# Kernel optimization log

Hardware: AMD Instinct MI355X
Metric: run time of the kernel (lower is better)

The kernel has to match this reference:

```python
import jax, jax.numpy as jnp
import numpy as np

N_NODES = 50000
N_EDGES = 600000
D = 128
EPS = 1e-5


def setup_inputs() -> dict:
    key = jax.random.key(0)
    ks = jax.random.split(key, 12)
    s = 1.0 / np.sqrt(D)
    return {
        "h": jax.random.normal(ks[0], (N_NODES, D), dtype=jnp.float32),
        "src": jax.random.randint(ks[1], (N_EDGES,), 0, N_NODES),
        "dst": jax.random.randint(ks[2], (N_EDGES,), 0, N_NODES),
        "W_pre": jax.random.uniform(ks[3], (D, D), jnp.float32, -s, s),
        "b_pre": jax.random.uniform(ks[4], (D,), jnp.float32, -s, s),
        "W1": jax.random.uniform(ks[5], (D, D), jnp.float32, -s, s),
        "b1": jax.random.uniform(ks[6], (D,), jnp.float32, -s, s),
        "W2": jax.random.uniform(ks[7], (D, D), jnp.float32, -s, s),
        "b2": jax.random.uniform(ks[8], (D,), jnp.float32, -s, s),
        "gamma": jnp.ones((D,), jnp.float32),
        "beta": jnp.zeros((D,), jnp.float32),
    }


def layer_norm(x, gamma, beta):
    mu = jnp.mean(x, axis=-1, keepdims=True)
    var = jnp.mean(jnp.square(x - mu), axis=-1, keepdims=True)
    return (x - mu) * jax.lax.rsqrt(var + EPS) * gamma + beta


def reference(h, src, dst, W_pre, b_pre, W1, b1, W2, b2, gamma, beta):
    # pre-projection: [N, D]
    h = h @ W_pre + b_pre
    # message passing: gather from src, segment-sum at dst (copy_u + sum)
    agg = jax.ops.segment_sum(h[src], dst, num_segments=N_NODES)
    # MLP (dropout is identity in eval)
    h_new = jax.nn.relu(jax.nn.relu(agg @ W1 + b1) @ W2 + b2)
    # residual + LayerNorm
    return layer_norm(h + h_new, gamma, beta)
```

## Files before the change

### kernel.cpp

```cpp
#include <hip/hip_runtime.h>

#define D 128
#define EPS 1e-5f
#define SCAN_CHUNK 1024
#define TSTRIDE 136

typedef __attribute__((ext_vector_type(8))) short bf16x8;
typedef __attribute__((ext_vector_type(4))) float floatx4;

__device__ __forceinline__ unsigned short f2bf(float f) {
    union { float f; unsigned u; } v; v.f = f;
    unsigned r = v.u + 0x7fffu + ((v.u >> 16) & 1u);
    return (unsigned short)(r >> 16);
}
__device__ __forceinline__ float bf2f(unsigned short s) {
    union { unsigned u; float f; } v; v.u = ((unsigned)s) << 16; return v.f;
}

__global__ __launch_bounds__(256) void prep(const float* __restrict__ W0,
                                            const float* __restrict__ W1,
                                            const float* __restrict__ W2,
                                            unsigned short* __restrict__ wt,
                                            int* __restrict__ counts,
                                            int* __restrict__ offsets, int nN, int nE) {
    int idx = blockIdx.x * 256 + threadIdx.x;
    if (idx < 3 * D * D) {
        int w = idx >> 14;
        int r = idx & (D * D - 1);
        int f = r >> 7, k = r & (D - 1);
        const float* W = (w == 0) ? W0 : (w == 1) ? W1 : W2;
        wt[(size_t)w * D * D + (size_t)f * D + k] = f2bf(W[(size_t)k * D + f]);
    }
    if (idx < nN) counts[idx] = 0;
    if (idx == 0) offsets[nN] = nE;
}

__global__ __launch_bounds__(256) void hist_dst(const int* __restrict__ dst,
                                                int* __restrict__ counts, int nE) {
    int e = blockIdx.x * 256 + threadIdx.x;
    if (e < nE) atomicAdd(&counts[dst[e]], 1);
}

__global__ __launch_bounds__(256) void scan_chunk_sums(const int* __restrict__ counts,
                                                       int* __restrict__ chunkSums, int n) {
    __shared__ int sh[256];
    const int t = threadIdx.x;
    const int base = blockIdx.x * SCAN_CHUNK + t * 4;
    int s = 0;
#pragma unroll
    for (int i = 0; i < 4; ++i) {
        int idx = base + i;
        if (idx < n) s += counts[idx];
    }
    sh[t] = s;
    __syncthreads();
    for (int off = 128; off > 0; off >>= 1) {
        if (t < off) sh[t] += sh[t + off];
        __syncthreads();
    }
    if (t == 0) chunkSums[blockIdx.x] = sh[0];
}

__global__ __launch_bounds__(256) void scan_final(const int* __restrict__ counts,
                                                  const int* __restrict__ chunkSums,
                                                  int nChunks,
                                                  int* __restrict__ offsets,
                                                  int* __restrict__ cursor, int n) {
    __shared__ int sh[256];
    __shared__ int sbase;
    const int t = threadIdx.x;
    if (t < 64) {
        int orig = (t < nChunks) ? chunkSums[t] : 0;
        int v = orig;
#pragma unroll
        for (int off = 1; off < 64; off <<= 1) {
            int u = __shfl_up(v, off, 64);
            if (t >= off) v += u;
        }
        if (t == blockIdx.x) sbase = v - orig;
    }
    const int base = blockIdx.x * SCAN_CHUNK + t * 4;
    int c[4];
    int s = 0;
#pragma unroll
    for (int i = 0; i < 4; ++i) {
        int idx = base + i;
        c[i] = (idx < n) ? counts[idx] : 0;
        s += c[i];
    }
    sh[t] = s;
    __syncthreads();
    int val = s;
    for (int off = 1; off < 256; off <<= 1) {
        int u = (t >= off) ? sh[t - off] : 0;
        __syncthreads();
        val += u;
        sh[t] = val;
        __syncthreads();
    }
    int run = val - s + sbase;
#pragma unroll
    for (int i = 0; i < 4; ++i) {
        int idx = base + i;
        if (idx < n) {
            offsets[idx] = run;
            cursor[idx] = run;
        }
        run += c[i];
    }
}

__global__ __launch_bounds__(256) void fill_edges(const int* __restrict__ src,
                                                  const int* __restrict__ dst,
                                                  int* __restrict__ cursor,
                                                  int* __restrict__ edge_src, int nE) {
    int e = blockIdx.x * 256 + threadIdx.x;
    if (e < nE) {
        int pos = atomicAdd(&cursor[dst[e]], 1);
        edge_src[pos] = src[e];
    }
}

__global__ __launch_bounds__(256) void gemm1(const float* __restrict__ X,
                                             const unsigned short* __restrict__ Wt,
                                             const float* __restrict__ bias,
                                             unsigned short* __restrict__ Y, int nrows) {
    const int t = threadIdx.x;
    const int lane = t & 63, wave = t >> 6;
    const int g = wave >> 1, hf = wave & 1;
    const int ml = lane & 15, q = lane >> 4;
    const int n0 = blockIdx.x * 64 + g * 32 + ml;
    const int n1 = n0 + 16;
    const int rr0 = (n0 < nrows) ? n0 : (nrows - 1);
    const int rr1 = (n1 < nrows) ? n1 : (nrows - 1);
    const bool ok0 = (n0 < nrows), ok1 = (n1 < nrows);

    bf16x8 bf0[4], bf1[4];
    {
        const float* x0 = X + (size_t)rr0 * D + q * 8;
        const float* x1 = X + (size_t)rr1 * D + q * 8;
#pragma unroll
        for (int kb = 0; kb < 4; ++kb) {
            float4 a0 = *(const float4*)(x0 + kb * 32);
            float4 a1 = *(const float4*)(x0 + kb * 32 + 4);
            float4 c0 = *(const float4*)(x1 + kb * 32);
            float4 c1 = *(const float4*)(x1 + kb * 32 + 4);
            bf16x8 v0, v1;
            v0[0] = (short)f2bf(a0.x); v0[1] = (short)f2bf(a0.y);
            v0[2] = (short)f2bf(a0.z); v0[3] = (short)f2bf(a0.w);
            v0[4] = (short)f2bf(a1.x); v0[5] = (short)f2bf(a1.y);
            v0[6] = (short)f2bf(a1.z); v0[7] = (short)f2bf(a1.w);
            v1[0] = (short)f2bf(c0.x); v1[1] = (short)f2bf(c0.y);
            v1[2] = (short)f2bf(c0.z); v1[3] = (short)f2bf(c0.w);
            v1[4] = (short)f2bf(c1.x); v1[5] = (short)f2bf(c1.y);
            v1[6] = (short)f2bf(c1.z); v1[7] = (short)f2bf(c1.w);
            bf0[kb] = v0; bf1[kb] = v1;
        }
    }

#pragma unroll
    for (int tl2 = 0; tl2 < 4; ++tl2) {
        const int tl = hf * 4 + tl2;
        floatx4 ac0 = {0.f, 0.f, 0.f, 0.f};
        floatx4 ac1 = {0.f, 0.f, 0.f, 0.f};
        const unsigned short* wp = Wt + (size_t)(tl * 16 + ml) * D + q * 8;
#pragma unroll
        for (int kb = 0; kb < 4; ++kb) {
            bf16x8 af = *(const bf16x8*)(wp + kb * 32);
            ac0 = __builtin_amdgcn_mfma_f32_16x16x32_bf16(af, bf0[kb], ac0, 0, 0, 0);
            ac1 = __builtin_amdgcn_mfma_f32_16x16x32_bf16(af, bf1[kb], ac1, 0, 0, 0);
        }
        const int f0i = tl * 16 + q * 4;
        float4 b4 = *(const float4*)(bias + f0i);
        if (ok0) {
            ushort4 o;
            o.x = f2bf(ac0[0] + b4.x); o.y = f2bf(ac0[1] + b4.y);
            o.z = f2bf(ac0[2] + b4.z); o.w = f2bf(ac0[3] + b4.w);
            *(ushort4*)(Y + (size_t)n0 * D + f0i) = o;
        }
        if (ok1) {
            ushort4 o;
            o.x = f2bf(ac1[0] + b4.x); o.y = f2bf(ac1[1] + b4.y);
            o.z = f2bf(ac1[2] + b4.z); o.w = f2bf(ac1[3] + b4.w);
            *(ushort4*)(Y + (size_t)n1 * D + f0i) = o;
        }
    }
}

__global__ __launch_bounds__(256) void gather_sum(const unsigned short* __restrict__ hpre,
                                                  const int* __restrict__ offsets,
                                                  const int* __restrict__ edge_src,
                                                  unsigned short* __restrict__ agg, int nN) {
    const int t = threadIdx.x;
    const int li = t & 15;
    const int n = blockIdx.x * 16 + (t >> 4);
    if (n >= nN) return;
    const int beg = offsets[n], end = offsets[n + 1];

    float a[8] = {0.f, 0.f, 0.f, 0.f, 0.f, 0.f, 0.f, 0.f};
    int j = beg;
    int s0 = 0, s1 = 0;
    if (j < end) s0 = edge_src[j];
    if (j + 1 < end) s1 = edge_src[j + 1];

    while (j + 1 < end) {
        const int c0 = s0, c1 = s1;
        const int jn = j + 2;
        if (jn < end) s0 = edge_src[jn];
        if (jn + 1 < end) s1 = edge_src[jn + 1];
        bf16x8 v0 = *(const bf16x8*)(hpre + (size_t)c0 * D + li * 8);
        bf16x8 v1 = *(const bf16x8*)(hpre + (size_t)c1 * D + li * 8);
#pragma unroll
        for (int i = 0; i < 8; ++i)
            a[i] += bf2f((unsigned short)v0[i]) + bf2f((unsigned short)v1[i]);
        j = jn;
    }
    if (j < end) {
        bf16x8 v0 = *(const bf16x8*)(hpre + (size_t)s0 * D + li * 8);
#pragma unroll
        for (int i = 0; i < 8; ++i) a[i] += bf2f((unsigned short)v0[i]);
    }

    bf16x8 p;
#pragma unroll
    for (int i = 0; i < 8; ++i) p[i] = (short)f2bf(a[i]);
    *(bf16x8*)(agg + (size_t)n * D + li * 8) = p;
}

__global__ __launch_bounds__(256) void fused_mlp(const unsigned short* __restrict__ agg,
                                                 const unsigned short* __restrict__ hpre,
                                                 const unsigned short* __restrict__ Wt1,
                                                 const float* __restrict__ b1,
                                                 const unsigned short* __restrict__ Wt2,
                                                 const float* __restrict__ b2,
                                                 const float* __restrict__ gamma,
                                                 const float* __restrict__ beta,
                                                 float* __restrict__ out, int nN) {
    __shared__ unsigned short tile[64 * TSTRIDE];
    __shared__ float psm[2][64], psq[2][64];
    const int t = threadIdx.x;
    const int lane = t & 63, wave = t >> 6;
    const int g = wave >> 1, hf = wave & 1;
    const int ml = lane & 15, q = lane >> 4;
    const int lr0 = g * 32 + ml, lr1 = lr0 + 16;
    const int n0 = blockIdx.x * 64 + lr0;
    const int n1 = blockIdx.x * 64 + lr1;
    const int rr0 = (n0 < nN) ? n0 : (nN - 1);
    const int rr1 = (n1 < nN) ? n1 : (nN - 1);
    const bool ok0 = (n0 < nN), ok1 = (n1 < nN);

    {
        bf16x8 bf0[4], bf1[4];
        const unsigned short* x0 = agg + (size_t)rr0 * D + q * 8;
        const unsigned short* x1 = agg + (size_t)rr1 * D + q * 8;
#pragma unroll
        for (int kb = 0; kb < 4; ++kb) {
            bf0[kb] = *(const bf16x8*)(x0 + kb * 32);
            bf1[kb] = *(const bf16x8*)(x1 + kb * 32);
        }

#pragma unroll
        for (int tl2 = 0; tl2 < 4; ++tl2) {
            const int tl = hf * 4 + tl2;
            floatx4 ac0 = {0.f, 0.f, 0.f, 0.f};
            floatx4 ac1 = {0.f, 0.f, 0.f, 0.f};
            const unsigned short* wp = Wt1 + (size_t)(tl * 16 + ml) * D + q * 8;
#pragma unroll
            for (int kb = 0; kb < 4; ++kb) {
                bf16x8 af = *(const bf16x8*)(wp + kb * 32);
                ac0 = __builtin_amdgcn_mfma_f32_16x16x32_bf16(af, bf0[kb], ac0, 0, 0, 0);
                ac1 = __builtin_amdgcn_mfma_f32_16x16x32_bf16(af, bf1[kb], ac1, 0, 0, 0);
            }
            const int f0i = tl * 16 + q * 4;
            float4 b4 = *(const float4*)(b1 + f0i);
            ushort4 o0, o1;
            o0.x = f2bf(fmaxf(ac0[0] + b4.x, 0.f));
            o0.y = f2bf(fmaxf(ac0[1] + b4.y, 0.f));
            o0.z = f2bf(fmaxf(ac0[2] + b4.z, 0.f));
            o0.w = f2bf(fmaxf(ac0[3] + b4.w, 0.f));
            o1.x = f2bf(fmaxf(ac1[0] + b4.x, 0.f));
            o1.y = f2bf(fmaxf(ac1[1] + b4.y, 0.f));
            o1.z = f2bf(fmaxf(ac1[2] + b4.z, 0.f));
            o1.w = f2bf(fmaxf(ac1[3] + b4.w, 0.f));
            *(ushort4*)(&tile[lr0 * TSTRIDE + f0i]) = o0;
            *(ushort4*)(&tile[lr1 * TSTRIDE + f0i]) = o1;
        }
    }
    __syncthreads();

    float vs0[4][4], vs1[4][4];
    {
        bf16x8 bf0[4], bf1[4];
#pragma unroll
        for (int kb = 0; kb < 4; ++kb) {
            bf0[kb] = *(const bf16x8*)(&tile[lr0 * TSTRIDE + kb * 32 + q * 8]);
            bf1[kb] = *(const bf16x8*)(&tile[lr1 * TSTRIDE + kb * 32 + q * 8]);
        }

        float sm0 = 0.f, sq0 = 0.f, sm1 = 0.f, sq1 = 0.f;
#pragma unroll
        for (int tl2 = 0; tl2 < 4; ++tl2) {
            const int tl = hf * 4 + tl2;
            floatx4 ac0 = {0.f, 0.f, 0.f, 0.f};
            floatx4 ac1 = {0.f, 0.f, 0.f, 0.f};
            const unsigned short* wp = Wt2 + (size_t)(tl * 16 + ml) * D + q * 8;
#pragma unroll
            for (int kb = 0; kb < 4; ++kb) {
                bf16x8 af = *(const bf16x8*)(wp + kb * 32);
                ac0 = __builtin_amdgcn_mfma_f32_16x16x32_bf16(af, bf0[kb], ac0, 0, 0, 0);
                ac1 = __builtin_amdgcn_mfma_f32_16x16x32_bf16(af, bf1[kb], ac1, 0, 0, 0);
            }
            const int f0i = tl * 16 + q * 4;
            float4 b4 = *(const float4*)(b2 + f0i);
            ushort4 h0 = ((const ushort4*)(hpre + (size_t)rr0 * D + f0i))[0];
            ushort4 h1 = ((const ushort4*)(hpre + (size_t)rr1 * D + f0i))[0];
            float a0 = fmaxf(ac0[0] + b4.x, 0.f) + bf2f(h0.x);
            float a1 = fmaxf(ac0[1] + b4.y, 0.f) + bf2f(h0.y);
            float a2 = fmaxf(ac0[2] + b4.z, 0.f) + bf2f(h0.z);
            float a3 = fmaxf(ac0[3] + b4.w, 0.f) + bf2f(h0.w);
            float c0 = fmaxf(ac1[0] + b4.x, 0.f) + bf2f(h1.x);
            float c1 = fmaxf(ac1[1] + b4.y, 0.f) + bf2f(h1.y);
            float c2 = fmaxf(ac1[2] + b4.z, 0.f) + bf2f(h1.z);
            float c3 = fmaxf(ac1[3] + b4.w, 0.f) + bf2f(h1.w);
            vs0[tl2][0] = a0; vs0[tl2][1] = a1; vs0[tl2][2] = a2; vs0[tl2][3] = a3;
            vs1[tl2][0] = c0; vs1[tl2][1] = c1; vs1[tl2][2] = c2; vs1[tl2][3] = c3;
            sm0 += a0 + a1 + a2 + a3;
            sq0 += a0 * a0 + a1 * a1 + a2 * a2 + a3 * a3;
            sm1 += c0 + c1 + c2 + c3;
            sq1 += c0 * c0 + c1 * c1 + c2 * c2 + c3 * c3;
        }
        sm0 += __shfl_xor(sm0, 16); sm0 += __shfl_xor(sm0, 32);
        sq0 += __shfl_xor(sq0, 16); sq0 += __shfl_xor(sq0, 32);
        sm1 += __shfl_xor(sm1, 16); sm1 += __shfl_xor(sm1, 32);
        sq1 += __shfl_xor(sq1, 16); sq1 += __shfl_xor(sq1, 32);
        if (lane < 16) {
            psm[hf][lr0] = sm0; psq[hf][lr0] = sq0;
            psm[hf][lr1] = sm1; psq[hf][lr1] = sq1;
        }
    }
    __syncthreads();

    {
        const float smT0 = psm[0][lr0] + psm[1][lr0];
        const float sqT0 = psq[0][lr0] + psq[1][lr0];
        const float smT1 = psm[0][lr1] + psm[1][lr1];
        const float sqT1 = psq[0][lr1] + psq[1][lr1];
        const float mu0 = smT0 * (1.f / D);
        const float is0 = rsqrtf(sqT0 * (1.f / D) - mu0 * mu0 + EPS);
        const float mu1 = smT1 * (1.f / D);
        const float is1 = rsqrtf(sqT1 * (1.f / D) - mu1 * mu1 + EPS);

#pragma unroll
        for (int tl2 = 0; tl2 < 4; ++tl2) {
            const int f0i = (hf * 4 + tl2) * 16 + q * 4;
            float4 g4 = *(const float4*)(gamma + f0i);
            float4 be4 = *(const float4*)(beta + f0i);
            if (ok0) {
                float4 o;
                o.x = (vs0[tl2][0] - mu0) * is0 * g4.x + be4.x;
                o.y = (vs0[tl2][1] - mu0) * is0 * g4.y + be4.y;
                o.z = (vs0[tl2][2] - mu0) * is0 * g4.z + be4.z;
                o.w = (vs0[tl2][3] - mu0) * is0 * g4.w + be4.w;
                *(float4*)(out + (size_t)n0 * D + f0i) = o;
            }
            if (ok1) {
                float4 o;
                o.x = (vs1[tl2][0] - mu1) * is1 * g4.x + be4.x;
                o.y = (vs1[tl2][1] - mu1) * is1 * g4.y + be4.y;
                o.z = (vs1[tl2][2] - mu1) * is1 * g4.z + be4.z;
                o.w = (vs1[tl2][3] - mu1) * is1 * g4.w + be4.w;
                *(float4*)(out + (size_t)n1 * D + f0i) = o;
            }
        }
    }
}

extern "C" void kernel_launch(void* const* d_in, const int* in_sizes, int n_in,
                              void* d_out, int out_size, void* d_ws, size_t ws_size,
                              hipStream_t stream) {
    const float* h     = (const float*)d_in[0];
    const int*   src   = (const int*)d_in[1];
    const int*   dst   = (const int*)d_in[2];
    const float* W_pre = (const float*)d_in[3];
    const float* b_pre = (const float*)d_in[4];
    const float* W1    = (const float*)d_in[5];
    const float* b1    = (const float*)d_in[6];
    const float* W2    = (const float*)d_in[7];
    const float* b2    = (const float*)d_in[8];
    const float* gamma = (const float*)d_in[9];
    const float* beta  = (const float*)d_in[10];
    float* out = (float*)d_out;

    const int nN = in_sizes[0] / D;
    const int nE = in_sizes[1];
    const size_t rowsz = (size_t)nN * D;

    unsigned short* hpre = (unsigned short*)d_ws;
    unsigned short* agg  = hpre + rowsz;
    unsigned short* wt   = agg + rowsz;
    int* edge_src  = (int*)(wt + 3 * D * D);
    int* offsets   = edge_src + nE;
    int* cursor    = offsets + nN + 1;
    int* counts    = cursor + nN;
    int* chunkSums = counts + nN;

    const int prep_n  = (3 * D * D > nN) ? 3 * D * D : nN;
    const int eblocks = (nE + 255) / 256;
    const int gblocks = (nN + 63) / 64;
    const int nChunks = (nN + SCAN_CHUNK - 1) / SCAN_CHUNK;

    prep<<<(prep_n + 255) / 256, 256, 0, stream>>>(W_pre, W1, W2, wt, counts, offsets, nN, nE);
    hist_dst<<<eblocks, 256, 0, stream>>>(dst, counts, nE);
    scan_chunk_sums<<<nChunks, 256, 0, stream>>>(counts, chunkSums, nN);
    scan_final<<<nChunks, 256, 0, stream>>>(counts, chunkSums, nChunks, offsets, cursor, nN);
    fill_edges<<<eblocks, 256, 0, stream>>>(src, dst, cursor, edge_src, nE);

    gemm1<<<gblocks, 256, 0, stream>>>(h, wt, b_pre, hpre, nN);
    gather_sum<<<(nN + 15) / 16, 256, 0, stream>>>(hpre, offsets, edge_src, agg, nN);
    fused_mlp<<<gblocks, 256, 0, stream>>>(agg, hpre, wt + D * D, b1, wt + 2 * D * D, b2,
                                           gamma, beta, out, nN);
}
```

Measured before the change: 227.5 us.

## Fuse histogram into gemm1, single-pass scan, fixed-point deterministic gather sum

The dst histogram is folded into the pre-projection GEMM launch, with every fourth block doing atomic counting while the others compute GEMM tiles. The two-kernel scan becomes one kernel in which each block recomputes its prefix by summing all earlier counts. The gather-sum now accumulates in 64-bit fixed point via llrintf, unrolled by four edges, giving an order-independent result. Together these remove two launches and overlap the histogram with the GEMM, at the cost of redundant prefix reads and more expensive integer conversion arithmetic in the gather loop.

Result: slower. 257.9 us (+13.4%).

```diff
diff --git a/kernel.cpp b/kernel.cpp
--- a/kernel.cpp
+++ b/kernel.cpp
@@ -4,6 +4,8 @@
 #define EPS 1e-5f
 #define SCAN_CHUNK 1024
 #define TSTRIDE 136
+#define FIXSCALE 1099511627776.0f
+#define INVFIXSCALE (1.0f / 1099511627776.0f)
 
 typedef __attribute__((ext_vector_type(8))) short bf16x8;
 typedef __attribute__((ext_vector_type(4))) float floatx4;
@@ -35,101 +37,31 @@
     if (idx == 0) offsets[nN] = nE;
 }
 
-__global__ __launch_bounds__(256) void hist_dst(const int* __restrict__ dst,
-                                                int* __restrict__ counts, int nE) {
-    int e = blockIdx.x * 256 + threadIdx.x;
-    if (e < nE) atomicAdd(&counts[dst[e]], 1);
-}
-
-__global__ __launch_bounds__(256) void scan_chunk_sums(const int* __restrict__ counts,
-                                                       int* __restrict__ chunkSums, int n) {
-    __shared__ int sh[256];
-    const int t = threadIdx.x;
-    const int base = blockIdx.x * SCAN_CHUNK + t * 4;
-    int s = 0;
-#pragma unroll
-    for (int i = 0; i < 4; ++i) {
-        int idx = base + i;
-        if (idx < n) s += counts[idx];
-    }
-    sh[t] = s;
-    __syncthreads();
-    for (int off = 128; off > 0; off >>= 1) {
-        if (t < off) sh[t] += sh[t + off];
-        __syncthreads();
-    }
-    if (t == 0) chunkSums[blockIdx.x] = sh[0];
-}
-
-__global__ __launch_bounds__(256) void scan_final(const int* __restrict__ counts,
-                                                  const int* __restrict__ chunkSums,
-                                                  int nChunks,
-                                                  int* __restrict__ offsets,
-                                                  int* __restrict__ cursor, int n) {
-    __shared__ int sh[256];
-    __shared__ int sbase;
-    const int t = threadIdx.x;
-    if (t < 64) {
-        int orig = (t < nChunks) ? chunkSums[t] : 0;
-        int v = orig;
-#pragma unroll
-        for (int off = 1; off < 64; off <<= 1) {
-            int u = __shfl_up(v, off, 64);
-            if (t >= off) v += u;
-        }
-        if (t == blockIdx.x) sbase = v - orig;
-    }
-    const int base = blockIdx.x * SCAN_CHUNK + t * 4;
-    int c[4];
-    int s = 0;
-#pragma unroll
-    for (int i = 0; i < 4; ++i) {
-        int idx = base + i;
-        c[i] = (idx < n) ? counts[idx] : 0;
-        s += c[i];
-    }
-    sh[t] = s;
-    __syncthreads();
-    int val = s;
-    for (int off = 1; off < 256; off <<= 1) {
-        int u = (t >= off) ? sh[t - off] : 0;
-        __syncthreads();
-        val += u;
-        sh[t] = val;
-        __syncthreads();
-    }
-    int run = val - s + sbase;
-#pragma unroll
-    for (int i = 0; i < 4; ++i) {
-        int idx = base + i;
-        if (idx < n) {
-            offsets[idx] = run;
-            cursor[idx] = run;
-        }
-        run += c[i];
-    }
-}
-
-__global__ __launch_bounds__(256) void fill_edges(const int* __restrict__ src,
+__global__ __launch_bounds__(256) void gemm1_hist(const float* __restrict__ X,
+                                                  const unsigned short* __restrict__ Wt,
+                                                  const float* __restrict__ bias,
+                                                  unsigned short* __restrict__ Y, int nrows,
                                                   const int* __restrict__ dst,
-                                                  int* __restrict__ cursor,
-                                                  int* __restrict__ edge_src, int nE) {
-    int e = blockIdx.x * 256 + threadIdx.x;
-    if (e < nE) {
-        int pos = atomicAdd(&cursor[dst[e]], 1);
-        edge_src[pos] = src[e];
-    }
-}
-
-__global__ __launch_bounds__(256) void gemm1(const float* __restrict__ X,
-                                             const unsigned short* __restrict__ Wt,
-                                             const float* __restrict__ bias,
-                                             unsigned short* __restrict__ Y, int nrows) {
+                                                  int* __restrict__ counts, int nE, int HB) {
+    const int bid = blockIdx.x;
+    const int r = bid >> 2, c = bid & 3;
+
+    if (c == 3) {
+        const int stride = HB * 256;
+        for (int e = r * 256 + threadIdx.x; e < nE; e += stride)
+            atomicAdd(&counts[dst[e]], 1);
+        return;
+    }
+
+    const int tile = 3 * r + c;
+    const int gblocks = (nrows + 63) / 64;
+    if (tile >= gblocks) return;
+
     const int t = threadIdx.x;
     const int lane = t & 63, wave = t >> 6;
     const int g = wave >> 1, hf = wave & 1;
     const int ml = lane & 15, q = lane >> 4;
-    const int n0 = blockIdx.x * 64 + g * 32 + ml;
+    const int n0 = tile * 64 + g * 32 + ml;
     const int n1 = n0 + 16;
     const int rr0 = (n0 < nrows) ? n0 : (nrows - 1);
     const int rr1 = (n1 < nrows) ? n1 : (nrows - 1);
@@ -187,6 +119,69 @@
     }
 }
 
+__global__ __launch_bounds__(256) void scan_all(const int* __restrict__ counts,
+                                                int* __restrict__ offsets,
+                                                int* __restrict__ cursor, int n) {
+    __shared__ int sh[256];
+    __shared__ int sbase_sh;
+    const int t = threadIdx.x;
+    const int base0 = blockIdx.x * SCAN_CHUNK;
+
+    int ps = 0;
+    for (int i = t; i < base0; i += 256) ps += counts[i];
+    sh[t] = ps;
+    __syncthreads();
+    for (int off = 128; off > 0; off >>= 1) {
+        if (t < off) sh[t] += sh[t + off];
+        __syncthreads();
+    }
+    if (t == 0) sbase_sh = sh[0];
+    __syncthreads();
+    const int sbase = sbase_sh;
+    __syncthreads();
+
+    const int base = base0 + t * 4;
+    int c[4];
+    int s = 0;
+#pragma unroll
+    for (int i = 0; i < 4; ++i) {
+        int idx = base + i;
+        c[i] = (idx < n) ? counts[idx] : 0;
+        s += c[i];
+    }
+    sh[t] = s;
+    __syncthreads();
+    int val = s;
+    for (int off = 1; off < 256; off <<= 1) {
+        int u = (t >= off) ? sh[t - off] : 0;
+        __syncthreads();
+        val += u;
+        sh[t] = val;
+        __syncthreads();
+    }
+    int run = val - s + sbase;
+#pragma unroll
+    for (int i = 0; i < 4; ++i) {
+        int idx = base + i;
+        if (idx < n) {
+            offsets[idx] = run;
+            cursor[idx] = run;
+        }
+        run += c[i];
+    }
+}
+
+__global__ __launch_bounds__(256) void fill_edges(const int* __restrict__ src,
+                                                  const int* __restrict__ dst,
+                                                  int* __restrict__ cursor,
+                                                  int* __restrict__ edge_src, int nE) {
+    int e = blockIdx.x * 256 + threadIdx.x;
+    if (e < nE) {
+        int pos = atomicAdd(&cursor[dst[e]], 1);
+        edge_src[pos] = src[e];
+    }
+}
+
 __global__ __launch_bounds__(256) void gather_sum(const unsigned short* __restrict__ hpre,
                                                   const int* __restrict__ offsets,
                                                   const int* __restrict__ edge_src,
@@ -197,33 +192,35 @@
     if (n >= nN) return;
     const int beg = offsets[n], end = offsets[n + 1];
 
-    float a[8] = {0.f, 0.f, 0.f, 0.f, 0.f, 0.f, 0.f, 0.f};
+    long long a[8] = {0, 0, 0, 0, 0, 0, 0, 0};
     int j = beg;
-    int s0 = 0, s1 = 0;
-    if (j < end) s0 = edge_src[j];
-    if (j + 1 < end) s1 = edge_src[j + 1];
-
-    while (j + 1 < end) {
-        const int c0 = s0, c1 = s1;
-        const int jn = j + 2;
-        if (jn < end) s0 = edge_src[jn];
-        if (jn + 1 < end) s1 = edge_src[jn + 1];
-        bf16x8 v0 = *(const bf16x8*)(hpre + (size_t)c0 * D + li * 8);
-        bf16x8 v1 = *(const bf16x8*)(hpre + (size_t)c1 * D + li * 8);
+    while (j + 4 <= end) {
+        const int i0 = edge_src[j], i1 = edge_src[j + 1];
+        const int i2 = edge_src[j + 2], i3 = edge_src[j + 3];
+        bf16x8 v0 = *(const bf16x8*)(hpre + (size_t)i0 * D + li * 8);
+        bf16x8 v1 = *(const bf16x8*)(hpre + (size_t)i1 * D + li * 8);
+        bf16x8 v2 = *(const bf16x8*)(hpre + (size_t)i2 * D + li * 8);
+        bf16x8 v3 = *(const bf16x8*)(hpre + (size_t)i3 * D + li * 8);
+#pragma unroll
+        for (int i = 0; i < 8; ++i) {
+            a[i] += llrintf(bf2f((unsigned short)v0[i]) * FIXSCALE)
+                  + llrintf(bf2f((unsigned short)v1[i]) * FIXSCALE)
+                  + llrintf(bf2f((unsigned short)v2[i]) * FIXSCALE)
+                  + llrintf(bf2f((unsigned short)v3[i]) * FIXSCALE);
+        }
+        j += 4;
+    }
+    while (j < end) {
+        const int i0 = edge_src[j++];
+        bf16x8 v0 = *(const bf16x8*)(hpre + (size_t)i0 * D + li * 8);
 #pragma unroll
         for (int i = 0; i < 8; ++i)
-            a[i] += bf2f((unsigned short)v0[i]) + bf2f((unsigned short)v1[i]);
-        j = jn;
-    }
-    if (j < end) {
-        bf16x8 v0 = *(const bf16x8*)(hpre + (size_t)s0 * D + li * 8);
-#pragma unroll
-        for (int i = 0; i < 8; ++i) a[i] += bf2f((unsigned short)v0[i]);
+            a[i] += llrintf(bf2f((unsigned short)v0[i]) * FIXSCALE);
     }
 
     bf16x8 p;
 #pragma unroll
-    for (int i = 0; i < 8; ++i) p[i] = (short)f2bf(a[i]);
+    for (int i = 0; i < 8; ++i) p[i] = (short)f2bf((float)a[i] * INVFIXSCALE);
     *(bf16x8*)(agg + (size_t)n * D + li * 8) = p;
 }
 
@@ -402,20 +399,18 @@
     int* offsets   = edge_src + nE;
     int* cursor    = offsets + nN + 1;
     int* counts    = cursor + nN;
-    int* chunkSums = counts + nN;
 
     const int prep_n  = (3 * D * D > nN) ? 3 * D * D : nN;
     const int eblocks = (nE + 255) / 256;
     const int gblocks = (nN + 63) / 64;
+    const int HB      = (gblocks + 2) / 3;
+    const int cgrid   = 4 * HB;
     const int nChunks = (nN + SCAN_CHUNK - 1) / SCAN_CHUNK;
 
     prep<<<(prep_n + 255) / 256, 256, 0, stream>>>(W_pre, W1, W2, wt, counts, offsets, nN, nE);
-    hist_dst<<<eblocks, 256, 0, stream>>>(dst, counts, nE);
-    scan_chunk_sums<<<nChunks, 256, 0, stream>>>(counts, chunkSums, nN);
-    scan_final<<<nChunks, 256, 0, stream>>>(counts, chunkSums, nChunks, offsets, cursor, nN);
+    gemm1_hist<<<cgrid, 256, 0, stream>>>(h, wt, b_pre, hpre, nN, dst, counts, nE, HB);
+    scan_all<<<nChunks, 256, 0, stream>>>(counts, offsets, cursor, nN);
     fill_edges<<<eblocks, 256, 0, stream>>>(src, dst, cursor, edge_src, nE);
-
-    gemm1<<<gblocks, 256, 0, stream>>>(h, wt, b_pre, hpre, nN);
     gather_sum<<<(nN + 15) / 16, 256, 0, stream>>>(hpre, offsets, edge_src, agg, nN);
     fused_mlp<<<gblocks, 256, 0, stream>>>(agg, hpre, wt + D * D, b1, wt + 2 * D * D, b2,
                                            gamma, beta, out, nN);
```
